# Kernel optimization log

Hardware: AMD Instinct MI355X
Metric: run time of the kernel (lower is better)

## Reference

```python
import jax, jax.numpy as jnp
import numpy as np

N_NODES = 50000
N_EDGES = 1600000
IN_FEAT = 256
HID = IN_FEAT // 2  # 128
OUT_FEAT = 256


def setup_inputs() -> dict:
    key = jax.random.key(0)
    ks = jax.random.split(key, 10)
    x = jax.random.normal(ks[0], (N_NODES, IN_FEAT), dtype=jnp.float32)
    w = jax.random.uniform(ks[1], (N_EDGES, 1), dtype=jnp.float32)
    src = jax.random.randint(ks[2], (N_EDGES,), 0, N_NODES, dtype=jnp.int32)
    dst = jax.random.randint(ks[3], (N_EDGES,), 0, N_NODES, dtype=jnp.int32)
    s = 1.0 / np.sqrt(IN_FEAT)
    W_node = jax.random.uniform(ks[4], (IN_FEAT, HID), jnp.float32, -s, s)
    b_node = jax.random.uniform(ks[5], (HID,), jnp.float32, -s, s)
    W_edge = jax.random.uniform(ks[6], (IN_FEAT, HID), jnp.float32, -s, s)
    b_edge = jax.random.uniform(ks[7], (HID,), jnp.float32, -s, s)
    s2 = 1.0 / np.sqrt(HID)
    W_mlp = jax.random.uniform(ks[8], (HID, OUT_FEAT), jnp.float32, -s2, s2)
    b_mlp = jax.random.uniform(ks[9], (OUT_FEAT,), jnp.float32, -s2, s2)
    return {"x": x, "w": w, "src": src, "dst": dst,
            "W_node": W_node, "b_node": b_node,
            "W_edge": W_edge, "b_edge": b_edge,
            "W_mlp": W_mlp, "b_mlp": b_mlp}


def reference(x, w, src, dst, W_node, b_node, W_edge, b_edge, W_mlp, b_mlp):
    # message[v] = sum_{(u->v) in E} x[u] * w_e   (src_mul_edge + sum)
    message = jax.ops.segment_sum(x[src] * w, dst, num_segments=x.shape[0])  # [N, in_feat]
    h = (x @ W_node + b_node) + (message @ W_edge + b_edge)  # [N, in_feat//2]
    # NOTE: original uses nn.LeakyReLU(True) -> negative_slope=1.0 (identity);
    # replicated faithfully.
    h = jax.nn.leaky_relu(h, negative_slope=1.0)
    return h @ W_mlp + b_mlp  # [N, out_feat]
```

## Files before the change

### kernel.cpp

```cpp
#include <hip/hip_runtime.h>


constexpr int N_NODES  = 50000;
constexpr int N_EDGES  = 1600000;
constexpr int IN_FEAT  = 256;
constexpr int HID      = 128;
constexpr int OUT_FEAT = 256;

constexpr int BIN_SZ   = 32;
constexpr int N_BINS   = (N_NODES + BIN_SZ - 1) / BIN_SZ;
constexpr int CAPBIN   = 1536;
constexpr int EPB      = 4096;
constexpr int N_CBLK   = (N_EDGES + EPB - 1) / EPB;

typedef __attribute__((ext_vector_type(8))) short bf16x8;
typedef __attribute__((ext_vector_type(8))) unsigned short u16x8;
typedef __attribute__((ext_vector_type(4))) float f32x4;

static __device__ __forceinline__ unsigned short f2bf(float f) {
    unsigned u = __builtin_bit_cast(unsigned, f);
    u += 0x7FFF + ((u >> 16) & 1);
    return (unsigned short)(u >> 16);
}
static __device__ __forceinline__ float bflo(unsigned u) {
    return __builtin_bit_cast(float, u << 16);
}
static __device__ __forceinline__ float bfhi(unsigned u) {
    return __builtin_bit_cast(float, u & 0xFFFF0000u);
}

__global__ __launch_bounds__(256) void k0_convert(
    const float* __restrict__ Wn, const float* __restrict__ We,
    const float* __restrict__ Wm,
    unsigned short* __restrict__ Wcat_t, unsigned short* __restrict__ Wmt)
{
    int n = blockIdx.x;
    int k = threadIdx.x;
    float v = (n < HID) ? Wn[(size_t)k * HID + n] : We[(size_t)k * HID + (n - HID)];
    Wcat_t[(size_t)n * IN_FEAT + k] = f2bf(v);
    if (k < HID) Wmt[(size_t)n * HID + k] = f2bf(Wm[(size_t)k * OUT_FEAT + n]);
}

__global__ __launch_bounds__(512) void binC(
    const int* __restrict__ src, const int* __restrict__ dst,
    const float* __restrict__ w, int* __restrict__ cursor,
    int2* __restrict__ entries)
{
    __shared__ int  hist[N_BINS];
    __shared__ int  gbase[N_BINS];
    __shared__ int  wsum[8];
    __shared__ int  stot;
    __shared__ int2 sorted[EPB];

    const int t = threadIdx.x;
    const int wave = t >> 6, lane = t & 63;
    const int e0 = blockIdx.x * EPB;

    for (int i = t; i < N_BINS; i += 512) hist[i] = 0;
    __syncthreads();

    int meta[8], wb[8], rk[8], bn[8];
    #pragma unroll
    for (int k = 0; k < 8; ++k) {
        int e = e0 + t + k * 512;
        bn[k] = -1;
        if (e < N_EDGES) {
            int d = dst[e];
            int b = d >> 5;
            bn[k]   = b;
            meta[k] = src[e] | ((d & 31) << 16) | (b << 21);
            wb[k]   = __float_as_int(w[e]);
            rk[k]   = atomicAdd(&hist[b], 1);
        }
    }
    __syncthreads();

    const int b4 = t * 4;
    int c0 = 0, c1 = 0, c2 = 0, c3 = 0;
    if (b4 + 0 < N_BINS) c0 = hist[b4 + 0];
    if (b4 + 1 < N_BINS) c1 = hist[b4 + 1];
    if (b4 + 2 < N_BINS) c2 = hist[b4 + 2];
    if (b4 + 3 < N_BINS) c3 = hist[b4 + 3];
    const int s = c0 + c1 + c2 + c3;
    int pre = s;
    #pragma unroll
    for (int off = 1; off < 64; off <<= 1) {
        int o = __shfl_up(pre, off, 64);
        if (lane >= off) pre += o;
    }
    if (lane == 63) wsum[wave] = pre;
    __syncthreads();
    if (t == 0) {
        int r = 0;
        #pragma unroll
        for (int q = 0; q < 8; ++q) { int v = wsum[q]; wsum[q] = r; r += v; }
        stot = r;
    }
    __syncthreads();
    const int tb = wsum[wave] + pre - s;

    if (b4 + 0 < N_BINS) {
        hist[b4 + 0]  = tb;
        gbase[b4 + 0] = c0 ? atomicAdd(&cursor[b4 + 0], c0) : 0;
    }
    if (b4 + 1 < N_BINS) {
        hist[b4 + 1]  = tb + c0;
        gbase[b4 + 1] = c1 ? atomicAdd(&cursor[b4 + 1], c1) : 0;
    }
    if (b4 + 2 < N_BINS) {
        hist[b4 + 2]  = tb + c0 + c1;
        gbase[b4 + 2] = c2 ? atomicAdd(&cursor[b4 + 2], c2) : 0;
    }
    if (b4 + 3 < N_BINS) {
        hist[b4 + 3]  = tb + c0 + c1 + c2;
        gbase[b4 + 3] = c3 ? atomicAdd(&cursor[b4 + 3], c3) : 0;
    }
    __syncthreads();

    #pragma unroll
    for (int k = 0; k < 8; ++k)
        if (bn[k] >= 0)
            sorted[hist[bn[k]] + rk[k]] = make_int2(meta[k], wb[k]);
    __syncthreads();

    const int tot = stot;
    #pragma unroll
    for (int k = 0; k < 8; ++k) {
        int i = t + k * 512;
        if (i < tot) {
            int2 q = sorted[i];
            int b = ((unsigned)q.x) >> 21;
            int r = i - hist[b];
            int g = gbase[b] + r;
            if (g < CAPBIN)
                entries[(size_t)b * CAPBIN + g] = make_int2(q.x & 0x1FFFFF, q.y);
        }
    }
}

__global__ __launch_bounds__(512) void gatherB(
    const unsigned short* __restrict__ ybf, const float* __restrict__ h0,
    const int* __restrict__ cursor, const int2* __restrict__ entries,
    unsigned short* __restrict__ hbf)
{
    __shared__ int2 sorted[CAPBIN];
    __shared__ int  cnt32[BIN_SZ];
    __shared__ int  offs32[BIN_SZ];

    const int t = threadIdx.x;
    const int bin = blockIdx.x;
    const int node0 = bin * BIN_SZ;
    const int wave = t >> 6, lane = t & 63;

    const int tot = min(cursor[bin], CAPBIN);
    if (t < BIN_SZ) cnt32[t] = 0;
    __syncthreads();

    int2 held[3];
    int  hrank[3], hdloc[3];
    #pragma unroll
    for (int k = 0; k < 3; ++k) {
        hdloc[k] = -1;
        int g = t + k * 512;
        if (g < tot) {
            int2 ep = entries[(size_t)bin * CAPBIN + g];
            int dloc = ep.x >> 16;
            held[k]  = make_int2(ep.x & 0xFFFF, ep.y);
            hdloc[k] = dloc;
            hrank[k] = atomicAdd(&cnt32[dloc], 1);
        }
    }
    __syncthreads();

    if (wave == 0) {
        int v = (lane < BIN_SZ) ? cnt32[lane] : 0;
        int sum = v;
        #pragma unroll
        for (int off = 1; off < BIN_SZ; off <<= 1) {
            int o = __shfl_up(sum, off, 64);
            if (lane >= off) sum += o;
        }
        if (lane < BIN_SZ) offs32[lane] = sum - v;
    }
    __syncthreads();

    #pragma unroll
    for (int k = 0; k < 3; ++k)
        if (hdloc[k] >= 0)
            sorted[offs32[hdloc[k]] + hrank[k]] = held[k];
    __syncthreads();

    #pragma unroll
    for (int n4 = 0; n4 < 4; ++n4) {
        const int nl = wave * 4 + n4;
        const int node = node0 + nl;
        const int beg = offs32[nl];
        const int c = cnt32[nl];
        float a0 = 0.f, a1 = 0.f;
        int j = 0;
        for (; j + 4 <= c; j += 4) {
            int2 q0 = sorted[beg + j];
            int2 q1 = sorted[beg + j + 1];
            int2 q2 = sorted[beg + j + 2];
            int2 q3 = sorted[beg + j + 3];
            unsigned u0 = *(const unsigned*)&ybf[(size_t)q0.x * HID + 2 * lane];
            unsigned u1 = *(const unsigned*)&ybf[(size_t)q1.x * HID + 2 * lane];
            unsigned u2 = *(const unsigned*)&ybf[(size_t)q2.x * HID + 2 * lane];
            unsigned u3 = *(const unsigned*)&ybf[(size_t)q3.x * HID + 2 * lane];
            float w0 = __int_as_float(q0.y), w1 = __int_as_float(q1.y);
            float w2 = __int_as_float(q2.y), w3 = __int_as_float(q3.y);
            a0 += w0 * bflo(u0); a1 += w0 * bfhi(u0);
            a0 += w1 * bflo(u1); a1 += w1 * bfhi(u1);
            a0 += w2 * bflo(u2); a1 += w2 * bfhi(u2);
            a0 += w3 * bflo(u3); a1 += w3 * bfhi(u3);
        }
        for (; j < c; ++j) {
            int2 q = sorted[beg + j];
            unsigned u = *(const unsigned*)&ybf[(size_t)q.x * HID + 2 * lane];
            float wq = __int_as_float(q.y);
            a0 += wq * bflo(u); a1 += wq * bfhi(u);
        }
        if (node < N_NODES) {
            float2 hv = *(const float2*)&h0[(size_t)node * HID + 2 * lane];
            unsigned r = ((unsigned)f2bf(hv.y + a1) << 16)
                       | (unsigned)f2bf(hv.x + a0);
            *(unsigned*)&hbf[(size_t)node * HID + 2 * lane] = r;
        }
    }
}

__global__ __launch_bounds__(256, 4) void gemm1(
    const float* __restrict__ x, const unsigned short* __restrict__ Wcat_t,
    const float* __restrict__ bn, const float* __restrict__ be,
    float* __restrict__ h0, unsigned short* __restrict__ ybf)
{
    __shared__ unsigned short As[128][64];
    __shared__ unsigned short Bs[128][64];
    const int t = threadIdx.x;
    const int m0 = blockIdx.x * 128;
    const int nhalf = blockIdx.y;
    const int n0r = nhalf * 128;

    const int wave = t >> 6, lane = t & 63;
    const int wm = wave & 1, wn = wave >> 1;
    const int la = lane & 15, kq = lane >> 4;

    f32x4 acc[4][4];
    const f32x4 zero = {0.f, 0.f, 0.f, 0.f};
    #pragma unroll
    for (int i = 0; i < 4; ++i)
        #pragma unroll
        for (int j = 0; j < 4; ++j) acc[i][j] = zero;

    const float4* xg = (const float4*)x;
    const int srow = t >> 3, sc8 = t & 7;

    for (int kt = 0; kt < 4; ++kt) {
        if (kt) __syncthreads();
        #pragma unroll
        for (int i = 0; i < 4; ++i) {
            int row = srow + i * 32;
            int node = m0 + row;
            float4 v0 = make_float4(0.f, 0.f, 0.f, 0.f), v1 = v0;
            if (node < N_NODES) {
                v0 = xg[(size_t)node * 64 + kt * 16 + sc8 * 2];
                v1 = xg[(size_t)node * 64 + kt * 16 + sc8 * 2 + 1];
            }
            u16x8 b;
            b[0] = f2bf(v0.x); b[1] = f2bf(v0.y); b[2] = f2bf(v0.z); b[3] = f2bf(v0.w);
            b[4] = f2bf(v1.x); b[5] = f2bf(v1.y); b[6] = f2bf(v1.z); b[7] = f2bf(v1.w);
            *(u16x8*)&As[row][(sc8 ^ (row & 7)) * 8] = b;
        }
        #pragma unroll
        for (int i = 0; i < 4; ++i) {
            int row = srow + i * 32;
            float4 v = *(const float4*)(
                Wcat_t + (size_t)(n0r + row) * IN_FEAT + kt * 64 + sc8 * 8);
            *(float4*)&Bs[row][(sc8 ^ (row & 7)) * 8] = v;
        }
        __syncthreads();

        #pragma unroll
        for (int ks = 0; ks < 2; ++ks) {
            bf16x8 a[4], b[4];
            #pragma unroll
            for (int i = 0; i < 4; ++i) {
                int row = wm * 64 + i * 16 + la;
                a[i] = *(const bf16x8*)&As[row][((ks * 4 + kq) ^ (row & 7)) * 8];
            }
            #pragma unroll
            for (int j = 0; j < 4; ++j) {
                int row = wn * 64 + j * 16 + la;
                b[j] = *(const bf16x8*)&Bs[row][((ks * 4 + kq) ^ (row & 7)) * 8];
            }
            #pragma unroll
            for (int i = 0; i < 4; ++i)
                #pragma unroll
                for (int j = 0; j < 4; ++j)
                    acc[i][j] = __builtin_amdgcn_mfma_f32_16x16x32_bf16(
                        a[i], b[j], acc[i][j], 0, 0, 0);
        }
    }

    float bias[4];
    if (nhalf == 0) {
        #pragma unroll
        for (int j = 0; j < 4; ++j) {
            int n = wn * 64 + j * 16 + la;
            bias[j] = bn[n] + be[n];
        }
    }
    #pragma unroll
    for (int i = 0; i < 4; ++i) {
        int mbase = m0 + wm * 64 + i * 16 + kq * 4;
        #pragma unroll
        for (int j = 0; j < 4; ++j) {
            int n = wn * 64 + j * 16 + la;
            #pragma unroll
            for (int r = 0; r < 4; ++r) {
                int m = mbase + r;
                if (m < N_NODES) {
                    if (nhalf == 0)
                        h0[(size_t)m * HID + n] = acc[i][j][r] + bias[j];
                    else
                        ybf[(size_t)m * HID + n] = f2bf(acc[i][j][r]);
                }
            }
        }
    }
}

__global__ __launch_bounds__(256, 4) void gemm2(
    const unsigned short* __restrict__ hbf, const unsigned short* __restrict__ Wmt,
    const float* __restrict__ bm, float* __restrict__ out)
{
    __shared__ unsigned short As[128][64];
    __shared__ unsigned short Bs[128][64];
    const int t = threadIdx.x;
    const int m0 = blockIdx.x * 128;
    const int n0 = blockIdx.y * 128;

    const int wave = t >> 6, lane = t & 63;
    const int wm = wave & 1, wn = wave >> 1;
    const int la = lane & 15, kq = lane >> 4;
    const int srow = t >> 3, sc8 = t & 7;

    f32x4 acc[4][4];
    const f32x4 zero = {0.f, 0.f, 0.f, 0.f};
    #pragma unroll
    for (int i = 0; i < 4; ++i)
        #pragma unroll
        for (int j = 0; j < 4; ++j) acc[i][j] = zero;

    for (int kt = 0; kt < 2; ++kt) {
        if (kt) __syncthreads();
        #pragma unroll
        for (int i = 0; i < 4; ++i) {
            int row = srow + i * 32;
            int node = m0 + row;
            if (node >= N_NODES) node = N_NODES - 1;
            float4 va = *(const float4*)(hbf + (size_t)node * HID + kt * 64 + sc8 * 8);
            float4 vb = *(const float4*)(Wmt + (size_t)(n0 + row) * HID + kt * 64 + sc8 * 8);
            *(float4*)&As[row][(sc8 ^ (row & 7)) * 8] = va;
            *(float4*)&Bs[row][(sc8 ^ (row & 7)) * 8] = vb;
        }
        __syncthreads();

        #pragma unroll
        for (int ks = 0; ks < 2; ++ks) {
            bf16x8 a[4], b[4];
            #pragma unroll
            for (int i = 0; i < 4; ++i) {
                int row = wm * 64 + i * 16 + la;
                a[i] = *(const bf16x8*)&As[row][((ks * 4 + kq) ^ (row & 7)) * 8];
            }
            #pragma unroll
            for (int j = 0; j < 4; ++j) {
                int row = wn * 64 + j * 16 + la;
                b[j] = *(const bf16x8*)&Bs[row][((ks * 4 + kq) ^ (row & 7)) * 8];
            }
            #pragma unroll
            for (int i = 0; i < 4; ++i)
                #pragma unroll
                for (int j = 0; j < 4; ++j)
                    acc[i][j] = __builtin_amdgcn_mfma_f32_16x16x32_bf16(
                        a[i], b[j], acc[i][j], 0, 0, 0);
        }
    }

    #pragma unroll
    for (int i = 0; i < 4; ++i) {
        int mbase = m0 + wm * 64 + i * 16 + kq * 4;
        #pragma unroll
        for (int j = 0; j < 4; ++j) {
            int n = n0 + wn * 64 + j * 16 + la;
            float b = bm[n];
            #pragma unroll
            for (int r = 0; r < 4; ++r) {
                int m = mbase + r;
                if (m < N_NODES)
                    out[(size_t)m * OUT_FEAT + n] = acc[i][j][r] + b;
            }
        }
    }
}

extern "C" void kernel_launch(void* const* d_in, const int* in_sizes, int n_in,
                              void* d_out, int out_size, void* d_ws, size_t ws_size,
                              hipStream_t stream) {
    const float* x   = (const float*)d_in[0];
    const float* w   = (const float*)d_in[1];
    const int*   src = (const int*)d_in[2];
    const int*   dst = (const int*)d_in[3];
    const float* Wn  = (const float*)d_in[4];
    const float* bn  = (const float*)d_in[5];
    const float* We  = (const float*)d_in[6];
    const float* be  = (const float*)d_in[7];
    const float* Wm  = (const float*)d_in[8];
    const float* bm  = (const float*)d_in[9];
    float* out = (float*)d_out;

    char* p = (char*)d_ws;
    float*          h0      = (float*)p;          p += (size_t)N_NODES * HID * 4;
    unsigned short* ybf     = (unsigned short*)p; p += (size_t)N_NODES * HID * 2;
    unsigned short* hbf     = (unsigned short*)p; p += (size_t)N_NODES * HID * 2;
    int2*           entries = (int2*)p;           p += (size_t)N_BINS * CAPBIN * 8;
    unsigned short* Wcat_t  = (unsigned short*)p; p += (size_t)256 * IN_FEAT * 2;
    unsigned short* Wmt     = (unsigned short*)p; p += (size_t)OUT_FEAT * HID * 2;
    int*            cursor  = (int*)p;            p += (size_t)N_BINS * 4;

    const int grid_m = (N_NODES + 127) / 128;
    dim3 blk(256);

    hipMemsetAsync(cursor, 0, (size_t)N_BINS * 4, stream);
    k0_convert<<<256, blk, 0, stream>>>(Wn, We, Wm, Wcat_t, Wmt);
    binC<<<N_CBLK, dim3(512), 0, stream>>>(src, dst, w, cursor, entries);
    gemm1<<<dim3(grid_m, 2), blk, 0, stream>>>(x, Wcat_t, bn, be, h0, ybf);
    gatherB<<<N_BINS, dim3(512), 0, stream>>>(ybf, h0, cursor, entries, hbf);
    gemm2<<<dim3(grid_m, 2), blk, 0, stream>>>(hbf, Wmt, bm, out);
}
```

Before: 268.8 us.

## Fuse edge binning and first GEMM into one horizontally-fused kernel

Merges the edge-binning kernel and the first node GEMM into a single launch, with block index selecting the role and shared memory overlaid through a union. The GEMM part is reworked for 512 threads (8 waves, each holding a 4x2 tile of MFMA accumulators) so that both roles share one block size. The aim is to overlap the atomic-heavy, memory-bound binning with the compute-bound GEMM and to save a launch gap. In exchange, the union means every block reserves shared memory for the larger binning layout, which can lower occupancy for GEMM blocks, and block scheduling order decides how much overlap actually happens.

```diff
diff --git a/kernel.cpp b/kernel.cpp
--- a/kernel.cpp
+++ b/kernel.cpp
@@ -12,6 +12,8 @@
 constexpr int CAPBIN   = 1536;
 constexpr int EPB      = 4096;
 constexpr int N_CBLK   = (N_EDGES + EPB - 1) / EPB;
+constexpr int GRID_M   = (N_NODES + 127) / 128;
+constexpr int N_G1BLK  = GRID_M * 2;
 
 typedef __attribute__((ext_vector_type(8))) short bf16x8;
 typedef __attribute__((ext_vector_type(8))) unsigned short u16x8;
@@ -41,99 +43,206 @@
     if (k < HID) Wmt[(size_t)n * HID + k] = f2bf(Wm[(size_t)k * OUT_FEAT + n]);
 }
 
-__global__ __launch_bounds__(512) void binC(
+union SharedU {
+    struct {
+        int  hist[N_BINS];
+        int  gbase[N_BINS];
+        int  wsum[8];
+        int  stot;
+        int2 sorted[EPB];
+    } bc;
+    struct {
+        unsigned short As[128][64];
+        unsigned short Bs[128][64];
+    } g1;
+};
+
+__global__ __launch_bounds__(512, 4) void fuse1(
     const int* __restrict__ src, const int* __restrict__ dst,
     const float* __restrict__ w, int* __restrict__ cursor,
-    int2* __restrict__ entries)
+    int2* __restrict__ entries,
+    const float* __restrict__ x, const unsigned short* __restrict__ Wcat_t,
+    const float* __restrict__ bn, const float* __restrict__ be,
+    float* __restrict__ h0, unsigned short* __restrict__ ybf)
 {
-    __shared__ int  hist[N_BINS];
-    __shared__ int  gbase[N_BINS];
-    __shared__ int  wsum[8];
-    __shared__ int  stot;
-    __shared__ int2 sorted[EPB];
-
+    __shared__ SharedU sh;
     const int t = threadIdx.x;
     const int wave = t >> 6, lane = t & 63;
-    const int e0 = blockIdx.x * EPB;
-
-    for (int i = t; i < N_BINS; i += 512) hist[i] = 0;
-    __syncthreads();
-
-    int meta[8], wb[8], rk[8], bn[8];
-    #pragma unroll
-    for (int k = 0; k < 8; ++k) {
-        int e = e0 + t + k * 512;
-        bn[k] = -1;
-        if (e < N_EDGES) {
-            int d = dst[e];
-            int b = d >> 5;
-            bn[k]   = b;
-            meta[k] = src[e] | ((d & 31) << 16) | (b << 21);
-            wb[k]   = __float_as_int(w[e]);
-            rk[k]   = atomicAdd(&hist[b], 1);
-        }
-    }
-    __syncthreads();
-
-    const int b4 = t * 4;
-    int c0 = 0, c1 = 0, c2 = 0, c3 = 0;
-    if (b4 + 0 < N_BINS) c0 = hist[b4 + 0];
-    if (b4 + 1 < N_BINS) c1 = hist[b4 + 1];
-    if (b4 + 2 < N_BINS) c2 = hist[b4 + 2];
-    if (b4 + 3 < N_BINS) c3 = hist[b4 + 3];
-    const int s = c0 + c1 + c2 + c3;
-    int pre = s;
-    #pragma unroll
-    for (int off = 1; off < 64; off <<= 1) {
-        int o = __shfl_up(pre, off, 64);
-        if (lane >= off) pre += o;
-    }
-    if (lane == 63) wsum[wave] = pre;
-    __syncthreads();
-    if (t == 0) {
-        int r = 0;
-        #pragma unroll
-        for (int q = 0; q < 8; ++q) { int v = wsum[q]; wsum[q] = r; r += v; }
-        stot = r;
-    }
-    __syncthreads();
-    const int tb = wsum[wave] + pre - s;
-
-    if (b4 + 0 < N_BINS) {
-        hist[b4 + 0]  = tb;
-        gbase[b4 + 0] = c0 ? atomicAdd(&cursor[b4 + 0], c0) : 0;
-    }
-    if (b4 + 1 < N_BINS) {
-        hist[b4 + 1]  = tb + c0;
-        gbase[b4 + 1] = c1 ? atomicAdd(&cursor[b4 + 1], c1) : 0;
-    }
-    if (b4 + 2 < N_BINS) {
-        hist[b4 + 2]  = tb + c0 + c1;
-        gbase[b4 + 2] = c2 ? atomicAdd(&cursor[b4 + 2], c2) : 0;
-    }
-    if (b4 + 3 < N_BINS) {
-        hist[b4 + 3]  = tb + c0 + c1 + c2;
-        gbase[b4 + 3] = c3 ? atomicAdd(&cursor[b4 + 3], c3) : 0;
-    }
-    __syncthreads();
-
-    #pragma unroll
-    for (int k = 0; k < 8; ++k)
-        if (bn[k] >= 0)
-            sorted[hist[bn[k]] + rk[k]] = make_int2(meta[k], wb[k]);
-    __syncthreads();
-
-    const int tot = stot;
-    #pragma unroll
-    for (int k = 0; k < 8; ++k) {
-        int i = t + k * 512;
-        if (i < tot) {
-            int2 q = sorted[i];
-            int b = ((unsigned)q.x) >> 21;
-            int r = i - hist[b];
-            int g = gbase[b] + r;
-            if (g < CAPBIN)
-                entries[(size_t)b * CAPBIN + g] = make_int2(q.x & 0x1FFFFF, q.y);
+
+    if (blockIdx.x < N_CBLK) {
+        const int e0 = blockIdx.x * EPB;
+
+        for (int i = t; i < N_BINS; i += 512) sh.bc.hist[i] = 0;
+        __syncthreads();
+
+        int meta[8], wb[8], rk[8], bin[8];
+        #pragma unroll
+        for (int k = 0; k < 8; ++k) {
+            int e = e0 + t + k * 512;
+            bin[k] = -1;
+            if (e < N_EDGES) {
+                int d = dst[e];
+                int b = d >> 5;
+                bin[k]  = b;
+                meta[k] = src[e] | ((d & 31) << 16) | (b << 21);
+                wb[k]   = __float_as_int(w[e]);
+                rk[k]   = atomicAdd(&sh.bc.hist[b], 1);
+            }
+        }
+        __syncthreads();
+
+        const int b4 = t * 4;
+        int c0 = 0, c1 = 0, c2 = 0, c3 = 0;
+        if (b4 + 0 < N_BINS) c0 = sh.bc.hist[b4 + 0];
+        if (b4 + 1 < N_BINS) c1 = sh.bc.hist[b4 + 1];
+        if (b4 + 2 < N_BINS) c2 = sh.bc.hist[b4 + 2];
+        if (b4 + 3 < N_BINS) c3 = sh.bc.hist[b4 + 3];
+        const int s = c0 + c1 + c2 + c3;
+        int pre = s;
+        #pragma unroll
+        for (int off = 1; off < 64; off <<= 1) {
+            int o = __shfl_up(pre, off, 64);
+            if (lane >= off) pre += o;
+        }
+        if (lane == 63) sh.bc.wsum[wave] = pre;
+        __syncthreads();
+        if (t == 0) {
+            int r = 0;
+            #pragma unroll
+            for (int q = 0; q < 8; ++q) { int v = sh.bc.wsum[q]; sh.bc.wsum[q] = r; r += v; }
+            sh.bc.stot = r;
+        }
+        __syncthreads();
+        const int tb = sh.bc.wsum[wave] + pre - s;
+
+        if (b4 + 0 < N_BINS) {
+            sh.bc.hist[b4 + 0]  = tb;
+            sh.bc.gbase[b4 + 0] = c0 ? atomicAdd(&cursor[b4 + 0], c0) : 0;
+        }
+        if (b4 + 1 < N_BINS) {
+            sh.bc.hist[b4 + 1]  = tb + c0;
+            sh.bc.gbase[b4 + 1] = c1 ? atomicAdd(&cursor[b4 + 1], c1) : 0;
+        }
+        if (b4 + 2 < N_BINS) {
+            sh.bc.hist[b4 + 2]  = tb + c0 + c1;
+            sh.bc.gbase[b4 + 2] = c2 ? atomicAdd(&cursor[b4 + 2], c2) : 0;
+        }
+        if (b4 + 3 < N_BINS) {
+            sh.bc.hist[b4 + 3]  = tb + c0 + c1 + c2;
+            sh.bc.gbase[b4 + 3] = c3 ? atomicAdd(&cursor[b4 + 3], c3) : 0;
+        }
+        __syncthreads();
+
+        #pragma unroll
+        for (int k = 0; k < 8; ++k)
+            if (bin[k] >= 0)
+                sh.bc.sorted[sh.bc.hist[bin[k]] + rk[k]] = make_int2(meta[k], wb[k]);
+        __syncthreads();
+
+        const int tot = sh.bc.stot;
+        #pragma unroll
+        for (int k = 0; k < 8; ++k) {
+            int i = t + k * 512;
+            if (i < tot) {
+                int2 q = sh.bc.sorted[i];
+                int b = ((unsigned)q.x) >> 21;
+                int r = i - sh.bc.hist[b];
+                int g = sh.bc.gbase[b] + r;
+                if (g < CAPBIN)
+                    entries[(size_t)b * CAPBIN + g] = make_int2(q.x & 0x1FFFFF, q.y);
+            }
+        }
+    } else {
+        const int bid2 = blockIdx.x - N_CBLK;
+        const int m0 = (bid2 >> 1) * 128;
+        const int nhalf = bid2 & 1;
+        const int n0r = nhalf * 128;
+
+        const int wm = wave >> 2, wn = wave & 3;
+        const int la = lane & 15, kq = lane >> 4;
+        const int srow = t >> 3, sc8 = t & 7;
+
+        f32x4 acc[4][2];
+        const f32x4 zero = {0.f, 0.f, 0.f, 0.f};
+        #pragma unroll
+        for (int i = 0; i < 4; ++i)
+            #pragma unroll
+            for (int j = 0; j < 2; ++j) acc[i][j] = zero;
+
+        const float4* xg = (const float4*)x;
+
+        for (int kt = 0; kt < 4; ++kt) {
+            if (kt) __syncthreads();
+            #pragma unroll
+            for (int i = 0; i < 2; ++i) {
+                int row = srow + i * 64;
+                int node = m0 + row;
+                float4 v0 = make_float4(0.f, 0.f, 0.f, 0.f), v1 = v0;
+                if (node < N_NODES) {
+                    v0 = xg[(size_t)node * 64 + kt * 16 + sc8 * 2];
+                    v1 = xg[(size_t)node * 64 + kt * 16 + sc8 * 2 + 1];
+                }
+                u16x8 b;
+                b[0] = f2bf(v0.x); b[1] = f2bf(v0.y); b[2] = f2bf(v0.z); b[3] = f2bf(v0.w);
+                b[4] = f2bf(v1.x); b[5] = f2bf(v1.y); b[6] = f2bf(v1.z); b[7] = f2bf(v1.w);
+                *(u16x8*)&sh.g1.As[row][(sc8 ^ (row & 7)) * 8] = b;
+            }
+            #pragma unroll
+            for (int i = 0; i < 2; ++i) {
+                int row = srow + i * 64;
+                float4 v = *(const float4*)(
+                    Wcat_t + (size_t)(n0r + row) * IN_FEAT + kt * 64 + sc8 * 8);
+                *(float4*)&sh.g1.Bs[row][(sc8 ^ (row & 7)) * 8] = v;
+            }
+            __syncthreads();
+
+            #pragma unroll
+            for (int ks = 0; ks < 2; ++ks) {
+                bf16x8 a[4], b[2];
+                #pragma unroll
+                for (int i = 0; i < 4; ++i) {
+                    int row = wm * 64 + i * 16 + la;
+                    a[i] = *(const bf16x8*)&sh.g1.As[row][((ks * 4 + kq) ^ (row & 7)) * 8];
+                }
+                #pragma unroll
+                for (int j = 0; j < 2; ++j) {
+                    int row = wn * 32 + j * 16 + la;
+                    b[j] = *(const bf16x8*)&sh.g1.Bs[row][((ks * 4 + kq) ^ (row & 7)) * 8];
+                }
+                #pragma unroll
+                for (int i = 0; i < 4; ++i)
+                    #pragma unroll
+                    for (int j = 0; j < 2; ++j)
+                        acc[i][j] = __builtin_amdgcn_mfma_f32_16x16x32_bf16(
+                            a[i], b[j], acc[i][j], 0, 0, 0);
+            }
+        }
+
+        float bias[2];
+        if (nhalf == 0) {
+            #pragma unroll
+            for (int j = 0; j < 2; ++j) {
+                int n = wn * 32 + j * 16 + la;
+                bias[j] = bn[n] + be[n];
+            }
+        }
+        #pragma unroll
+        for (int i = 0; i < 4; ++i) {
+            int mbase = m0 + wm * 64 + i * 16 + kq * 4;
+            #pragma unroll
+            for (int j = 0; j < 2; ++j) {
+                int n = wn * 32 + j * 16 + la;
+                #pragma unroll
+                for (int r = 0; r < 4; ++r) {
+                    int m = mbase + r;
+                    if (m < N_NODES) {
+                        if (nhalf == 0)
+                            h0[(size_t)m * HID + n] = acc[i][j][r] + bias[j];
+                        else
+                            ybf[(size_t)m * HID + n] = f2bf(acc[i][j][r]);
+                    }
+                }
+            }
         }
     }
 }
@@ -229,107 +338,6 @@
     }
 }
 
-__global__ __launch_bounds__(256, 4) void gemm1(
-    const float* __restrict__ x, const unsigned short* __restrict__ Wcat_t,
-    const float* __restrict__ bn, const float* __restrict__ be,
-    float* __restrict__ h0, unsigned short* __restrict__ ybf)
-{
-    __shared__ unsigned short As[128][64];
-    __shared__ unsigned short Bs[128][64];
-    const int t = threadIdx.x;
-    const int m0 = blockIdx.x * 128;
-    const int nhalf = blockIdx.y;
-    const int n0r = nhalf * 128;
-
-    const int wave = t >> 6, lane = t & 63;
-    const int wm = wave & 1, wn = wave >> 1;
-    const int la = lane & 15, kq = lane >> 4;
-
-    f32x4 acc[4][4];
-    const f32x4 zero = {0.f, 0.f, 0.f, 0.f};
-    #pragma unroll
-    for (int i = 0; i < 4; ++i)
-        #pragma unroll
-        for (int j = 0; j < 4; ++j) acc[i][j] = zero;
-
-    const float4* xg = (const float4*)x;
-    const int srow = t >> 3, sc8 = t & 7;
-
-    for (int kt = 0; kt < 4; ++kt) {
-        if (kt) __syncthreads();
-        #pragma unroll
-        for (int i = 0; i < 4; ++i) {
-            int row = srow + i * 32;
-            int node = m0 + row;
-            float4 v0 = make_float4(0.f, 0.f, 0.f, 0.f), v1 = v0;
-            if (node < N_NODES) {
-                v0 = xg[(size_t)node * 64 + kt * 16 + sc8 * 2];
-                v1 = xg[(size_t)node * 64 + kt * 16 + sc8 * 2 + 1];
-            }
-            u16x8 b;
-            b[0] = f2bf(v0.x); b[1] = f2bf(v0.y); b[2] = f2bf(v0.z); b[3] = f2bf(v0.w);
-            b[4] = f2bf(v1.x); b[5] = f2bf(v1.y); b[6] = f2bf(v1.z); b[7] = f2bf(v1.w);
-            *(u16x8*)&As[row][(sc8 ^ (row & 7)) * 8] = b;
-        }
-        #pragma unroll
-        for (int i = 0; i < 4; ++i) {
-            int row = srow + i * 32;
-            float4 v = *(const float4*)(
-                Wcat_t + (size_t)(n0r + row) * IN_FEAT + kt * 64 + sc8 * 8);
-            *(float4*)&Bs[row][(sc8 ^ (row & 7)) * 8] = v;
-        }
-        __syncthreads();
-
-        #pragma unroll
-        for (int ks = 0; ks < 2; ++ks) {
-            bf16x8 a[4], b[4];
-            #pragma unroll
-            for (int i = 0; i < 4; ++i) {
-                int row = wm * 64 + i * 16 + la;
-                a[i] = *(const bf16x8*)&As[row][((ks * 4 + kq) ^ (row & 7)) * 8];
-            }
-            #pragma unroll
-            for (int j = 0; j < 4; ++j) {
-                int row = wn * 64 + j * 16 + la;
-                b[j] = *(const bf16x8*)&Bs[row][((ks * 4 + kq) ^ (row & 7)) * 8];
-            }
-            #pragma unroll
-            for (int i = 0; i < 4; ++i)
-                #pragma unroll
-                for (int j = 0; j < 4; ++j)
-                    acc[i][j] = __builtin_amdgcn_mfma_f32_16x16x32_bf16(
-                        a[i], b[j], acc[i][j], 0, 0, 0);
-        }
-    }
-
-    float bias[4];
-    if (nhalf == 0) {
-        #pragma unroll
-        for (int j = 0; j < 4; ++j) {
-            int n = wn * 64 + j * 16 + la;
-            bias[j] = bn[n] + be[n];
-        }
-    }
-    #pragma unroll
-    for (int i = 0; i < 4; ++i) {
-        int mbase = m0 + wm * 64 + i * 16 + kq * 4;
-        #pragma unroll
-        for (int j = 0; j < 4; ++j) {
-            int n = wn * 64 + j * 16 + la;
-            #pragma unroll
-            for (int r = 0; r < 4; ++r) {
-                int m = mbase + r;
-                if (m < N_NODES) {
-                    if (nhalf == 0)
-                        h0[(size_t)m * HID + n] = acc[i][j][r] + bias[j];
-                    else
-                        ybf[(size_t)m * HID + n] = f2bf(acc[i][j][r]);
-                }
-            }
-        }
-    }
-}
-
 __global__ __launch_bounds__(256, 4) void gemm2(
     const unsigned short* __restrict__ hbf, const unsigned short* __restrict__ Wmt,
     const float* __restrict__ bm, float* __restrict__ out)
@@ -429,13 +437,12 @@
     unsigned short* Wmt     = (unsigned short*)p; p += (size_t)OUT_FEAT * HID * 2;
     int*            cursor  = (int*)p;            p += (size_t)N_BINS * 4;
 
-    const int grid_m = (N_NODES + 127) / 128;
     dim3 blk(256);
 
     hipMemsetAsync(cursor, 0, (size_t)N_BINS * 4, stream);
     k0_convert<<<256, blk, 0, stream>>>(Wn, We, Wm, Wcat_t, Wmt);
-    binC<<<N_CBLK, dim3(512), 0, stream>>>(src, dst, w, cursor, entries);
-    gemm1<<<dim3(grid_m, 2), blk, 0, stream>>>(x, Wcat_t, bn, be, h0, ybf);
+    fuse1<<<N_CBLK + N_G1BLK, dim3(512), 0, stream>>>(
+        src, dst, w, cursor, entries, x, Wcat_t, bn, be, h0, ybf);
     gatherB<<<N_BINS, dim3(512), 0, stream>>>(ybf, h0, cursor, entries, hbf);
-    gemm2<<<dim3(grid_m, 2), blk, 0, stream>>>(hbf, Wmt, bm, out);
-}
+    gemm2<<<dim3(GRID_M, 2), blk, 0, stream>>>(hbf, Wmt, bm, out);
+}
```

Result: faster. 250.8 us (-6.7%).
